# Optimization experiments

Hardware: AMD Instinct MI355X
Metric: run time of the kernel (lower is better)

Reference implementation:

```python
import jax, jax.numpy as jnp
import numpy as np

PAD = 1
K = 3  # kernel_size


def conv2d(x, w, b):
    y = jax.lax.conv_general_dilated(
        x, w, window_strides=(1, 1), padding=((PAD, PAD), (PAD, PAD)),
        dimension_numbers=("NCHW", "OIHW", "NCHW"))
    return y + b[None, :, None, None]


def deform_conv2d(x, offset, weight, bias):
    # torchvision.ops.deform_conv2d semantics (stride=1, dilation=1, 1 offset group)
    B, C, H, W = x.shape
    O = weight.shape[0]
    K2 = K * K
    off = offset.reshape(B, K2, 2, H, W)  # [...,0]=dy, [...,1]=dx
    ky, kx = jnp.meshgrid(jnp.arange(K), jnp.arange(K), indexing="ij")
    ky = ky.reshape(K2).astype(x.dtype)
    kx = kx.reshape(K2).astype(x.dtype)
    hh = jnp.arange(H, dtype=x.dtype)
    ww = jnp.arange(W, dtype=x.dtype)
    # sampling coords, shape [B, K2, H, W]
    py = off[:, :, 0] + ky[None, :, None, None] + hh[None, None, :, None] - PAD
    px = off[:, :, 1] + kx[None, :, None, None] + ww[None, None, None, :] - PAD

    y0 = jnp.floor(py)
    x0 = jnp.floor(px)
    wy = (py - y0)[:, None]  # [B,1,K2,H,W]
    wx = (px - x0)[:, None]

    xf = x.reshape(B, C, H * W)

    def gather(iy, ix):
        valid = (iy >= 0) & (iy < H) & (ix >= 0) & (ix < W)
        iyc = jnp.clip(iy, 0, H - 1).astype(jnp.int32)
        ixc = jnp.clip(ix, 0, W - 1).astype(jnp.int32)
        idx = (iyc * W + ixc).reshape(B, 1, K2 * H * W)
        v = jnp.take_along_axis(xf, idx, axis=2).reshape(B, C, K2, H, W)
        return v * valid.reshape(B, 1, K2, H, W).astype(x.dtype)

    v00 = gather(y0, x0)
    v01 = gather(y0, x0 + 1)
    v10 = gather(y0 + 1, x0)
    v11 = gather(y0 + 1, x0 + 1)
    sampled = (v00 * (1 - wy) * (1 - wx) + v01 * (1 - wy) * wx
               + v10 * wy * (1 - wx) + v11 * wy * wx)  # [B,C,K2,H,W]
    out = jnp.einsum("bckhw,ock->bohw", sampled, weight.reshape(O, C, K2))
    return out + bias[None, :, None, None]


def setup_inputs() -> dict:
    key = jax.random.key(0)
    k1, k2, k3, k4, k5 = jax.random.split(key, 5)
    B, C, H, W = 4, 64, 192, 192
    O = 64
    x = jax.random.normal(k1, (B, C, H, W), dtype=jnp.float32)
    w_off = jax.random.normal(k2, (2 * K * K, C, K, K), dtype=jnp.float32) * 0.05
    b_off = jnp.zeros((2 * K * K,), dtype=jnp.float32)
    w_conv = jax.random.normal(k3, (O, C, K, K), dtype=jnp.float32) * (1.0 / np.sqrt(C * K * K))
    b_conv = jax.random.normal(k4, (O,), dtype=jnp.float32) * 0.01
    return {"x": x, "w_off": w_off, "b_off": b_off, "w_conv": w_conv, "b_conv": b_conv}


def reference(x, w_off, b_off, w_conv, b_conv):
    offset = conv2d(x, w_off, b_off)
    y = deform_conv2d(x, offset, w_conv, b_conv)
    return conv2d(y, w_conv, b_conv)  # module reuses self.conv on deform output
```

## Files before the change

kernel.cpp:

```cpp
#include <hip/hip_runtime.h>

constexpr int B = 4;
constexpr int C = 64;
constexpr int O = 64;
constexpr int OOFF = 18;
constexpr int H = 192;
constexpr int W = 192;

typedef __attribute__((ext_vector_type(8))) short short8;
typedef __attribute__((ext_vector_type(4))) float float4v;
typedef __attribute__((ext_vector_type(2))) float f32x2;
typedef __attribute__((ext_vector_type(2))) uint u32x2;
typedef __attribute__((ext_vector_type(2))) __bf16 bf16x2;

__device__ inline ushort f2bf(float f) {
  return __builtin_bit_cast(ushort, (__bf16)f);
}
__device__ inline uint pk2bf(float lo, float hi) {
  bf16x2 v;
  v.x = (__bf16)lo;
  v.y = (__bf16)hi;
  return __builtin_bit_cast(uint, v);
}
__device__ inline f32x2 upk(uint u) {
  u32x2 t;
  t.x = u << 16;
  t.y = u & 0xffff0000u;
  return __builtin_bit_cast(f32x2, t);
}

__global__ __launch_bounds__(256) void k_pre(const float* __restrict__ x,
                                             ushort* __restrict__ xtb,
                                             const float* __restrict__ w_conv,
                                             ushort* __restrict__ wBf,
                                             const float* __restrict__ w_off,
                                             ushort* __restrict__ wOf) {
  __shared__ float tile[64][17];
  const int bid = blockIdx.x;
  const int tid = threadIdx.x;
  if (bid < 9216) {
    const int w0 = (bid % 12) * 16;
    const int h = (bid / 12) % 192;
    const int b = bid / 2304;
    const int wl = tid & 15;
    const int c0 = tid >> 4;
#pragma unroll
    for (int r = 0; r < 4; ++r) {
      const int c = c0 + r * 16;
      tile[c][wl] = x[(((size_t)b * C + c) * H + h) * W + w0 + wl];
    }
    __syncthreads();
    const int c = tid & 63;
    const int qq = tid >> 6;
#pragma unroll
    for (int r = 0; r < 4; ++r) {
      const int wq = qq + r * 4;
      xtb[(((size_t)b * H + h) * W + w0 + wq) * C + c] = f2bf(tile[c][wq]);
    }
  } else if (bid < 9360) {
    const int i = (bid - 9216) * 256 + tid;
    const int j = i & 7;
    const int lane = (i >> 3) & 63;
    const int nt = (i >> 9) & 3;
    const int kstep = (i >> 11) & 1;
    const int kk = i >> 12;
    const int n = nt + 4 * (lane & 15);
    const int c = kstep * 32 + ((lane >> 4) & 3) * 8 + j;
    wBf[i] = f2bf(w_conv[((size_t)n * C + c) * 9 + kk]);
  } else {
    const int i = (bid - 9360) * 256 + tid;
    const int j = i & 7;
    const int lane = (i >> 3) & 63;
    const int nt = (i >> 9) & 1;
    const int ks = (i >> 10) & 1;
    const int kk = i >> 11;
    const int n = nt * 16 + (lane & 15);
    const int c = ks * 32 + ((lane >> 4) & 3) * 8 + j;
    wOf[i] = (n < OOFF) ? f2bf(w_off[((size_t)n * C + c) * 9 + kk]) : (ushort)0;
  }
}

__global__ __launch_bounds__(256) void k_fused(
    const ushort* __restrict__ xtb, const ushort* __restrict__ wOf,
    const float* __restrict__ b_off, const ushort* __restrict__ wBf,
    const float* __restrict__ b_conv, ushort* __restrict__ yt) {
  __shared__ ushort sA[4][2][64][8];
  __shared__ __align__(16) float offBuf[4][16][20];

  const int bid = blockIdx.x;
  const int xcd = bid & 7;
  const int s = bid >> 3;
  const int b = xcd >> 1;
  const int half = xcd & 1;
  const int th = half * 12 + s / 24;
  const int tw = s % 24;
  const int h0 = th * 8, w0 = tw * 8;

  const int tid = threadIdx.x;
  const int wave = tid >> 6, lane = tid & 63;
  const int col = lane & 15, quad = lane >> 4;
  const int p = tid >> 2, qtr = tid & 3;
  const int pl = p & 15;
  const int prow = p >> 3, pcol = p & 7;
  const int h = h0 + prow, w = w0 + pcol;
  const int ks_w = qtr >> 1;
  const int q2 = (qtr & 1) * 2;

  {
    float4v oacc[2];
#pragma unroll
    for (int nt = 0; nt < 2; ++nt) oacc[nt] = (float4v){0.f, 0.f, 0.f, 0.f};

    short8 obfr[2][2][2];
    short8 oafr[2][2];

    auto oload = [&](int kk, int pb) {
      const int ky = kk / 3, kx = kk % 3;
      const int hh = h0 + 2 * wave + (col >> 3) + ky - 1;
      const int ww = w0 + (col & 7) + kx - 1;
      const bool ok = ((unsigned)hh < (unsigned)H) && ((unsigned)ww < (unsigned)W);
      const int hhc = min(max(hh, 0), H - 1);
      const int wwc = min(max(ww, 0), W - 1);
      const ushort* pa = xtb + (((size_t)b * H + hhc) * W + wwc) * C + quad * 8;
#pragma unroll
      for (int ks = 0; ks < 2; ++ks) {
        short8 v = (short8)0;
        if (ok) v = *(const short8*)(pa + ks * 32);
        oafr[pb][ks] = v;
#pragma unroll
        for (int nt = 0; nt < 2; ++nt)
          obfr[pb][ks][nt] = *(const short8*)&wOf[((((size_t)kk * 2 + ks) * 2 + nt) * 64 + lane) * 8];
      }
    };

    oload(0, 0);
#pragma unroll
    for (int kk = 0; kk < 9; ++kk) {
      const int pb = kk & 1;
      if (kk < 8) oload(kk + 1, pb ^ 1);
#pragma unroll
      for (int ks = 0; ks < 2; ++ks)
#pragma unroll
        for (int nt = 0; nt < 2; ++nt)
          oacc[nt] = __builtin_amdgcn_mfma_f32_16x16x32_bf16(oafr[pb][ks], obfr[pb][ks][nt],
                                                             oacc[nt], 0, 0, 0);
    }

#pragma unroll
    for (int nt = 0; nt < 2; ++nt) {
      const int oc = nt * 16 + col;
      if (oc < OOFF) {
        const float bias = b_off[oc];
#pragma unroll
        for (int r = 0; r < 4; ++r)
          offBuf[wave][quad * 4 + r][oc] = oacc[nt][r] + bias;
      }
    }
  }

  const ushort* xb = xtb + (size_t)b * H * W * C + qtr * 16;

  uint4 G[2][8];
  float4 aw[2];

  auto issue = [&](int kk, int buf) {
    const float2 ov = *(const float2*)&offBuf[wave][pl][2 * kk];
    const float dy = ov.x, dx = ov.y;
    const int ky = kk / 3, kx = kk % 3;
    const float pyf = dy + (float)(ky + h - 1);
    const float pxf = dx + (float)(kx + w - 1);
    const float fy0 = floorf(pyf), fx0 = floorf(pxf);
    const float wy = pyf - fy0, wx = pxf - fx0;
    const int iy0 = (int)fy0, ix0 = (int)fx0;
    const int iy1 = iy0 + 1, ix1 = ix0 + 1;
    const bool vy0 = (unsigned)iy0 < (unsigned)H;
    const bool vy1 = (unsigned)iy1 < (unsigned)H;
    const bool vx0 = (unsigned)ix0 < (unsigned)W;
    const bool vx1 = (unsigned)ix1 < (unsigned)W;
    aw[buf].x = (vy0 && vx0) ? (1.f - wy) * (1.f - wx) : 0.f;
    aw[buf].y = (vy0 && vx1) ? (1.f - wy) * wx : 0.f;
    aw[buf].z = (vy1 && vx0) ? wy * (1.f - wx) : 0.f;
    aw[buf].w = (vy1 && vx1) ? wy * wx : 0.f;
    const int cy0 = min(max(iy0, 0), H - 1), cy1 = min(max(iy1, 0), H - 1);
    const int cx0 = min(max(ix0, 0), W - 1), cx1 = min(max(ix1, 0), W - 1);
    const uint4* p00 = (const uint4*)(xb + ((size_t)cy0 * W + cx0) * C);
    const uint4* p01 = (const uint4*)(xb + ((size_t)cy0 * W + cx1) * C);
    const uint4* p10 = (const uint4*)(xb + ((size_t)cy1 * W + cx0) * C);
    const uint4* p11 = (const uint4*)(xb + ((size_t)cy1 * W + cx1) * C);
    G[buf][0] = p00[0]; G[buf][1] = p00[1];
    G[buf][2] = p01[0]; G[buf][3] = p01[1];
    G[buf][4] = p10[0]; G[buf][5] = p10[1];
    G[buf][6] = p11[0]; G[buf][7] = p11[1];
  };

  float4v acc[4];
#pragma unroll
  for (int nt = 0; nt < 4; ++nt) acc[nt] = (float4v){0.f, 0.f, 0.f, 0.f};

  issue(0, 0);
#pragma unroll
  for (int kk = 0; kk < 9; ++kk) {
    const int buf = kk & 1;
    if (kk < 8) issue(kk + 1, buf ^ 1);

    const f32x2 a00 = {aw[buf].x, aw[buf].x};
    const f32x2 a01 = {aw[buf].y, aw[buf].y};
    const f32x2 a10 = {aw[buf].z, aw[buf].z};
    const f32x2 a11 = {aw[buf].w, aw[buf].w};
    uint pk[8];
#pragma unroll
    for (int i = 0; i < 8; ++i) {
      const uint u00 = ((const uint*)&G[buf][0])[i];
      const uint u01 = ((const uint*)&G[buf][2])[i];
      const uint u10 = ((const uint*)&G[buf][4])[i];
      const uint u11 = ((const uint*)&G[buf][6])[i];
      f32x2 sv = upk(u00) * a00 + upk(u01) * a01 + upk(u10) * a10 + upk(u11) * a11;
      pk[i] = pk2bf(sv.x, sv.y);
    }
    *(uint4*)&sA[wave][ks_w][pl | (q2 << 4)][0] = *(const uint4*)&pk[0];
    *(uint4*)&sA[wave][ks_w][pl | ((q2 + 1) << 4)][0] = *(const uint4*)&pk[4];

#pragma unroll
    for (int ks = 0; ks < 2; ++ks) {
      const short8 a = *(const short8*)&sA[wave][ks][lane][0];
#pragma unroll
      for (int nt = 0; nt < 4; ++nt) {
        const short8 bb = *(const short8*)&wBf[((((size_t)kk * 2 + ks) * 4 + nt) * 64 + lane) * 8];
        acc[nt] = __builtin_amdgcn_mfma_f32_16x16x32_bf16(a, bb, acc[nt], 0, 0, 0);
      }
    }
  }

  float bias[4];
#pragma unroll
  for (int nt = 0; nt < 4; ++nt) bias[nt] = b_conv[4 * col + nt];
#pragma unroll
  for (int r = 0; r < 4; ++r) {
    const int pp = wave * 16 + quad * 4 + r;
    const int hrow = h0 + (pp >> 3), wcol = w0 + (pp & 7);
    uint2 u;
    u.x = pk2bf(acc[0][r] + bias[0], acc[1][r] + bias[1]);
    u.y = pk2bf(acc[2][r] + bias[2], acc[3][r] + bias[3]);
    *(uint2*)&yt[((size_t)(b * H + hrow) * W + wcol) * C + 4 * col] = u;
  }
}

__global__ __launch_bounds__(256) void k_conv_main_mfma(
    const ushort* __restrict__ yt, const ushort* __restrict__ wBf,
    const float* __restrict__ b_conv, float* __restrict__ out) {
  const int w0 = blockIdx.x * 16;
  const int b = blockIdx.z;
  const int tid = threadIdx.x;
  const int wave = tid >> 6, lane = tid & 63;
  const int col = lane & 15, quad = lane >> 4;
  const int h0 = blockIdx.y * 8 + wave * 2;

  float4v acc[2][4];
#pragma unroll
  for (int mt = 0; mt < 2; ++mt)
#pragma unroll
    for (int nt = 0; nt < 4; ++nt) acc[mt][nt] = (float4v){0.f, 0.f, 0.f, 0.f};

  short8 bfr[2][2][4];
  short8 afr[2][2][2];

  auto load = [&](int kk, int pb) {
    const int ky = kk / 3, kx = kk % 3;
    const int ww = w0 + col + kx - 1;
    const bool wok = (unsigned)ww < (unsigned)W;
    const int wwc = min(max(ww, 0), W - 1);
#pragma unroll
    for (int ks = 0; ks < 2; ++ks)
#pragma unroll
      for (int nt = 0; nt < 4; ++nt)
        bfr[pb][ks][nt] = *(const short8*)&wBf[((((size_t)kk * 2 + ks) * 4 + nt) * 64 + lane) * 8];
#pragma unroll
    for (int mt = 0; mt < 2; ++mt) {
      const int hh = h0 + mt + ky - 1;
      const bool ok = wok && ((unsigned)hh < (unsigned)H);
      const int hhc = min(max(hh, 0), H - 1);
      const ushort* pa = yt + (((size_t)b * H + hhc) * W + wwc) * C + quad * 8;
#pragma unroll
      for (int ks = 0; ks < 2; ++ks) {
        short8 v = (short8)0;
        if (ok) v = *(const short8*)(pa + ks * 32);
        afr[pb][mt][ks] = v;
      }
    }
  };

  load(0, 0);
#pragma unroll
  for (int kk = 0; kk < 9; ++kk) {
    const int pb = kk & 1;
    if (kk < 8) load(kk + 1, pb ^ 1);
#pragma unroll
    for (int ks = 0; ks < 2; ++ks)
#pragma unroll
      for (int mt = 0; mt < 2; ++mt)
#pragma unroll
        for (int nt = 0; nt < 4; ++nt)
          acc[mt][nt] = __builtin_amdgcn_mfma_f32_16x16x32_bf16(afr[pb][mt][ks], bfr[pb][ks][nt],
                                                                acc[mt][nt], 0, 0, 0);
  }

  float bias[4];
#pragma unroll
  for (int nt = 0; nt < 4; ++nt) bias[nt] = b_conv[4 * col + nt];
#pragma unroll
  for (int mt = 0; mt < 2; ++mt) {
    const int h = h0 + mt;
#pragma unroll
    for (int nt = 0; nt < 4; ++nt) {
      const int oc = 4 * col + nt;
      float4 v;
      v.x = acc[mt][nt][0] + bias[nt];
      v.y = acc[mt][nt][1] + bias[nt];
      v.z = acc[mt][nt][2] + bias[nt];
      v.w = acc[mt][nt][3] + bias[nt];
      *(float4*)&out[(((size_t)b * O + oc) * H + h) * W + w0 + quad * 4] = v;
    }
  }
}

extern "C" void kernel_launch(void* const* d_in, const int* in_sizes, int n_in,
                              void* d_out, int out_size, void* d_ws, size_t ws_size,
                              hipStream_t stream) {
  const float* x = (const float*)d_in[0];
  const float* w_off = (const float*)d_in[1];
  const float* b_off = (const float*)d_in[2];
  const float* w_conv = (const float*)d_in[3];
  const float* b_conv = (const float*)d_in[4];
  float* out = (float*)d_out;

  ushort* xtb = (ushort*)d_ws;
  ushort* yt = xtb + (size_t)B * H * W * C;
  ushort* wBf = yt + (size_t)B * H * W * C;
  ushort* wOf = wBf + 36864;

  const dim3 blk(256);
  k_pre<<<dim3(9432), blk, 0, stream>>>(x, xtb, w_conv, wBf, w_off, wOf);
  k_fused<<<dim3(2304), blk, 0, stream>>>(xtb, wOf, b_off, wBf, b_conv, yt);
  k_conv_main_mfma<<<dim3(W / 16, H / 8, B), blk, 0, stream>>>(yt, wBf, b_conv, out);
}
```

Before: 197.6 us.

## Switch intermediates to fp16, deepen gather prefetch, enlarge final conv tile

All intermediate tensors and weights move from bf16 to fp16, and the MFMAs switch to their f16 variants. Bilinear interpolation now runs in packed half arithmetic instead of unpacking to fp32, which cuts ALU work in the gather loop. The offsets are read into registers once, and the gather prefetch gets three buffers so loads run two steps ahead. The final conv doubles the rows per wave, giving more weight reuse per block but higher register pressure; fp16 interpolation also risks precision or overflow issues.

```diff
diff --git a/kernel.cpp b/kernel.cpp
--- a/kernel.cpp
+++ b/kernel.cpp
@@ -7,30 +7,22 @@
 constexpr int H = 192;
 constexpr int W = 192;
 
-typedef __attribute__((ext_vector_type(8))) short short8;
+typedef __attribute__((ext_vector_type(8))) _Float16 half8;
+typedef __attribute__((ext_vector_type(2))) _Float16 h16x2;
 typedef __attribute__((ext_vector_type(4))) float float4v;
-typedef __attribute__((ext_vector_type(2))) float f32x2;
-typedef __attribute__((ext_vector_type(2))) uint u32x2;
-typedef __attribute__((ext_vector_type(2))) __bf16 bf16x2;
-
-__device__ inline ushort f2bf(float f) {
-  return __builtin_bit_cast(ushort, (__bf16)f);
-}
-__device__ inline uint pk2bf(float lo, float hi) {
-  bf16x2 v;
-  v.x = (__bf16)lo;
-  v.y = (__bf16)hi;
+
+__device__ inline ushort f2h(float f) {
+  return __builtin_bit_cast(ushort, (_Float16)f);
+}
+__device__ inline uint pk2h(float lo, float hi) {
+  h16x2 v;
+  v.x = (_Float16)lo;
+  v.y = (_Float16)hi;
   return __builtin_bit_cast(uint, v);
 }
-__device__ inline f32x2 upk(uint u) {
-  u32x2 t;
-  t.x = u << 16;
-  t.y = u & 0xffff0000u;
-  return __builtin_bit_cast(f32x2, t);
-}
 
 __global__ __launch_bounds__(256) void k_pre(const float* __restrict__ x,
-                                             ushort* __restrict__ xtb,
+                                             ushort* __restrict__ xtf,
                                              const float* __restrict__ w_conv,
                                              ushort* __restrict__ wBf,
                                              const float* __restrict__ w_off,
@@ -55,7 +47,7 @@
 #pragma unroll
     for (int r = 0; r < 4; ++r) {
       const int wq = qq + r * 4;
-      xtb[(((size_t)b * H + h) * W + w0 + wq) * C + c] = f2bf(tile[c][wq]);
+      xtf[(((size_t)b * H + h) * W + w0 + wq) * C + c] = f2h(tile[c][wq]);
     }
   } else if (bid < 9360) {
     const int i = (bid - 9216) * 256 + tid;
@@ -66,7 +58,7 @@
     const int kk = i >> 12;
     const int n = nt + 4 * (lane & 15);
     const int c = kstep * 32 + ((lane >> 4) & 3) * 8 + j;
-    wBf[i] = f2bf(w_conv[((size_t)n * C + c) * 9 + kk]);
+    wBf[i] = f2h(w_conv[((size_t)n * C + c) * 9 + kk]);
   } else {
     const int i = (bid - 9360) * 256 + tid;
     const int j = i & 7;
@@ -76,12 +68,12 @@
     const int kk = i >> 11;
     const int n = nt * 16 + (lane & 15);
     const int c = ks * 32 + ((lane >> 4) & 3) * 8 + j;
-    wOf[i] = (n < OOFF) ? f2bf(w_off[((size_t)n * C + c) * 9 + kk]) : (ushort)0;
+    wOf[i] = (n < OOFF) ? f2h(w_off[((size_t)n * C + c) * 9 + kk]) : (ushort)0;
   }
 }
 
 __global__ __launch_bounds__(256) void k_fused(
-    const ushort* __restrict__ xtb, const ushort* __restrict__ wOf,
+    const ushort* __restrict__ xtf, const ushort* __restrict__ wOf,
     const float* __restrict__ b_off, const ushort* __restrict__ wBf,
     const float* __restrict__ b_conv, ushort* __restrict__ yt) {
   __shared__ ushort sA[4][2][64][8];
@@ -111,8 +103,8 @@
 #pragma unroll
     for (int nt = 0; nt < 2; ++nt) oacc[nt] = (float4v){0.f, 0.f, 0.f, 0.f};
 
-    short8 obfr[2][2][2];
-    short8 oafr[2][2];
+    half8 obfr[2][2][2];
+    half8 oafr[2][2];
 
     auto oload = [&](int kk, int pb) {
       const int ky = kk / 3, kx = kk % 3;
@@ -121,15 +113,15 @@
       const bool ok = ((unsigned)hh < (unsigned)H) && ((unsigned)ww < (unsigned)W);
       const int hhc = min(max(hh, 0), H - 1);
       const int wwc = min(max(ww, 0), W - 1);
-      const ushort* pa = xtb + (((size_t)b * H + hhc) * W + wwc) * C + quad * 8;
+      const ushort* pa = xtf + (((size_t)b * H + hhc) * W + wwc) * C + quad * 8;
 #pragma unroll
       for (int ks = 0; ks < 2; ++ks) {
-        short8 v = (short8)0;
-        if (ok) v = *(const short8*)(pa + ks * 32);
+        half8 v = (half8)0;
+        if (ok) v = *(const half8*)(pa + ks * 32);
         oafr[pb][ks] = v;
 #pragma unroll
         for (int nt = 0; nt < 2; ++nt)
-          obfr[pb][ks][nt] = *(const short8*)&wOf[((((size_t)kk * 2 + ks) * 2 + nt) * 64 + lane) * 8];
+          obfr[pb][ks][nt] = *(const half8*)&wOf[((((size_t)kk * 2 + ks) * 2 + nt) * 64 + lane) * 8];
       }
     };
 
@@ -142,8 +134,8 @@
       for (int ks = 0; ks < 2; ++ks)
 #pragma unroll
         for (int nt = 0; nt < 2; ++nt)
-          oacc[nt] = __builtin_amdgcn_mfma_f32_16x16x32_bf16(oafr[pb][ks], obfr[pb][ks][nt],
-                                                             oacc[nt], 0, 0, 0);
+          oacc[nt] = __builtin_amdgcn_mfma_f32_16x16x32_f16(oafr[pb][ks], obfr[pb][ks][nt],
+                                                            oacc[nt], 0, 0, 0);
     }
 
 #pragma unroll
@@ -158,14 +150,17 @@
     }
   }
 
-  const ushort* xb = xtb + (size_t)b * H * W * C + qtr * 16;
-
-  uint4 G[2][8];
-  float4 aw[2];
+  float2 offv[9];
+#pragma unroll
+  for (int kk = 0; kk < 9; ++kk) offv[kk] = *(const float2*)&offBuf[wave][pl][2 * kk];
+
+  const ushort* xb = xtf + (size_t)b * H * W * C + qtr * 16;
+
+  uint4 G[3][8];
+  float4 aw[3];
 
   auto issue = [&](int kk, int buf) {
-    const float2 ov = *(const float2*)&offBuf[wave][pl][2 * kk];
-    const float dy = ov.x, dx = ov.y;
+    const float dy = offv[kk].x, dx = offv[kk].y;
     const int ky = kk / 3, kx = kk % 3;
     const float pyf = dy + (float)(ky + h - 1);
     const float pxf = dx + (float)(kx + w - 1);
@@ -198,35 +193,35 @@
   for (int nt = 0; nt < 4; ++nt) acc[nt] = (float4v){0.f, 0.f, 0.f, 0.f};
 
   issue(0, 0);
+  issue(1, 1);
 #pragma unroll
   for (int kk = 0; kk < 9; ++kk) {
-    const int buf = kk & 1;
-    if (kk < 8) issue(kk + 1, buf ^ 1);
-
-    const f32x2 a00 = {aw[buf].x, aw[buf].x};
-    const f32x2 a01 = {aw[buf].y, aw[buf].y};
-    const f32x2 a10 = {aw[buf].z, aw[buf].z};
-    const f32x2 a11 = {aw[buf].w, aw[buf].w};
+    const int buf = kk % 3;
+    if (kk < 7) issue(kk + 2, (kk + 2) % 3);
+
+    const _Float16 w00 = (_Float16)aw[buf].x, w01 = (_Float16)aw[buf].y;
+    const _Float16 w10 = (_Float16)aw[buf].z, w11 = (_Float16)aw[buf].w;
+    const h16x2 a00 = {w00, w00}, a01 = {w01, w01}, a10 = {w10, w10}, a11 = {w11, w11};
     uint pk[8];
 #pragma unroll
     for (int i = 0; i < 8; ++i) {
-      const uint u00 = ((const uint*)&G[buf][0])[i];
-      const uint u01 = ((const uint*)&G[buf][2])[i];
-      const uint u10 = ((const uint*)&G[buf][4])[i];
-      const uint u11 = ((const uint*)&G[buf][6])[i];
-      f32x2 sv = upk(u00) * a00 + upk(u01) * a01 + upk(u10) * a10 + upk(u11) * a11;
-      pk[i] = pk2bf(sv.x, sv.y);
+      const h16x2 v00 = __builtin_bit_cast(h16x2, ((const uint*)&G[buf][0])[i]);
+      const h16x2 v01 = __builtin_bit_cast(h16x2, ((const uint*)&G[buf][2])[i]);
+      const h16x2 v10 = __builtin_bit_cast(h16x2, ((const uint*)&G[buf][4])[i]);
+      const h16x2 v11 = __builtin_bit_cast(h16x2, ((const uint*)&G[buf][6])[i]);
+      const h16x2 sv = v00 * a00 + v01 * a01 + v10 * a10 + v11 * a11;
+      pk[i] = __builtin_bit_cast(uint, sv);
     }
     *(uint4*)&sA[wave][ks_w][pl | (q2 << 4)][0] = *(const uint4*)&pk[0];
     *(uint4*)&sA[wave][ks_w][pl | ((q2 + 1) << 4)][0] = *(const uint4*)&pk[4];
 
 #pragma unroll
     for (int ks = 0; ks < 2; ++ks) {
-      const short8 a = *(const short8*)&sA[wave][ks][lane][0];
+      const half8 a = *(const half8*)&sA[wave][ks][lane][0];
 #pragma unroll
       for (int nt = 0; nt < 4; ++nt) {
-        const short8 bb = *(const short8*)&wBf[((((size_t)kk * 2 + ks) * 4 + nt) * 64 + lane) * 8];
-        acc[nt] = __builtin_amdgcn_mfma_f32_16x16x32_bf16(a, bb, acc[nt], 0, 0, 0);
+        const half8 bb = *(const half8*)&wBf[((((size_t)kk * 2 + ks) * 4 + nt) * 64 + lane) * 8];
+        acc[nt] = __builtin_amdgcn_mfma_f32_16x16x32_f16(a, bb, acc[nt], 0, 0, 0);
       }
     }
   }
@@ -239,8 +234,8 @@
     const int pp = wave * 16 + quad * 4 + r;
     const int hrow = h0 + (pp >> 3), wcol = w0 + (pp & 7);
     uint2 u;
-    u.x = pk2bf(acc[0][r] + bias[0], acc[1][r] + bias[1]);
-    u.y = pk2bf(acc[2][r] + bias[2], acc[3][r] + bias[3]);
+    u.x = pk2h(acc[0][r] + bias[0], acc[1][r] + bias[1]);
+    u.y = pk2h(acc[2][r] + bias[2], acc[3][r] + bias[3]);
     *(uint2*)&yt[((size_t)(b * H + hrow) * W + wcol) * C + 4 * col] = u;
   }
 }
@@ -253,16 +248,16 @@
   const int tid = threadIdx.x;
   const int wave = tid >> 6, lane = tid & 63;
   const int col = lane & 15, quad = lane >> 4;
-  const int h0 = blockIdx.y * 8 + wave * 2;
-
-  float4v acc[2][4];
-#pragma unroll
-  for (int mt = 0; mt < 2; ++mt)
+  const int h0 = blockIdx.y * 16 + wave * 4;
+
+  float4v acc[4][4];
+#pragma unroll
+  for (int mt = 0; mt < 4; ++mt)
 #pragma unroll
     for (int nt = 0; nt < 4; ++nt) acc[mt][nt] = (float4v){0.f, 0.f, 0.f, 0.f};
 
-  short8 bfr[2][2][4];
-  short8 afr[2][2][2];
+  half8 bfr[2][2][4];
+  half8 afr[2][4][2];
 
   auto load = [&](int kk, int pb) {
     const int ky = kk / 3, kx = kk % 3;
@@ -273,17 +268,17 @@
     for (int ks = 0; ks < 2; ++ks)
 #pragma unroll
       for (int nt = 0; nt < 4; ++nt)
-        bfr[pb][ks][nt] = *(const short8*)&wBf[((((size_t)kk * 2 + ks) * 4 + nt) * 64 + lane) * 8];
-#pragma unroll
-    for (int mt = 0; mt < 2; ++mt) {
+        bfr[pb][ks][nt] = *(const half8*)&wBf[((((size_t)kk * 2 + ks) * 4 + nt) * 64 + lane) * 8];
+#pragma unroll
+    for (int mt = 0; mt < 4; ++mt) {
       const int hh = h0 + mt + ky - 1;
       const bool ok = wok && ((unsigned)hh < (unsigned)H);
       const int hhc = min(max(hh, 0), H - 1);
       const ushort* pa = yt + (((size_t)b * H + hhc) * W + wwc) * C + quad * 8;
 #pragma unroll
       for (int ks = 0; ks < 2; ++ks) {
-        short8 v = (short8)0;
-        if (ok) v = *(const short8*)(pa + ks * 32);
+        half8 v = (half8)0;
+        if (ok) v = *(const half8*)(pa + ks * 32);
         afr[pb][mt][ks] = v;
       }
     }
@@ -297,18 +292,18 @@
 #pragma unroll
     for (int ks = 0; ks < 2; ++ks)
 #pragma unroll
-      for (int mt = 0; mt < 2; ++mt)
+      for (int mt = 0; mt < 4; ++mt)
 #pragma unroll
         for (int nt = 0; nt < 4; ++nt)
-          acc[mt][nt] = __builtin_amdgcn_mfma_f32_16x16x32_bf16(afr[pb][mt][ks], bfr[pb][ks][nt],
-                                                                acc[mt][nt], 0, 0, 0);
+          acc[mt][nt] = __builtin_amdgcn_mfma_f32_16x16x32_f16(afr[pb][mt][ks], bfr[pb][ks][nt],
+                                                               acc[mt][nt], 0, 0, 0);
   }
 
   float bias[4];
 #pragma unroll
   for (int nt = 0; nt < 4; ++nt) bias[nt] = b_conv[4 * col + nt];
 #pragma unroll
-  for (int mt = 0; mt < 2; ++mt) {
+  for (int mt = 0; mt < 4; ++mt) {
     const int h = h0 + mt;
 #pragma unroll
     for (int nt = 0; nt < 4; ++nt) {
@@ -333,13 +328,13 @@
   const float* b_conv = (const float*)d_in[4];
   float* out = (float*)d_out;
 
-  ushort* xtb = (ushort*)d_ws;
-  ushort* yt = xtb + (size_t)B * H * W * C;
+  ushort* xtf = (ushort*)d_ws;
+  ushort* yt = xtf + (size_t)B * H * W * C;
   ushort* wBf = yt + (size_t)B * H * W * C;
   ushort* wOf = wBf + 36864;
 
   const dim3 blk(256);
-  k_pre<<<dim3(9432), blk, 0, stream>>>(x, xtb, w_conv, wBf, w_off, wOf);
-  k_fused<<<dim3(2304), blk, 0, stream>>>(xtb, wOf, b_off, wBf, b_conv, yt);
-  k_conv_main_mfma<<<dim3(W / 16, H / 8, B), blk, 0, stream>>>(yt, wBf, b_conv, out);
-}
+  k_pre<<<dim3(9432), blk, 0, stream>>>(x, xtf, w_conv, wBf, w_off, wOf);
+  k_fused<<<dim3(2304), blk, 0, stream>>>(xtf, wOf, b_off, wBf, b_conv, yt);
+  k_conv_main_mfma<<<dim3(W / 16, H / 16, B), blk, 0, stream>>>(yt, wBf, b_conv, out);
+}
```

Result: slower. 203.3 us (+2.9%).
